# Performance work log

Hardware: AMD Instinct MI355X
Metric: run time of the kernel (lower is better)

Reference implementation:

```python
import jax, jax.numpy as jnp
import numpy as np

B, P1, P2 = 32, 25, 24          # batch, patch rows (+1 cls row), patch cols
D1, D2, D3 = 8, 8, 12           # factored embed dims (total d = 768)
H1, H2, H3 = 2, 2, 4            # factored heads (16 total)
X, Y, Z = D1 // H1, D2 // H2, D3 // H3   # per-head factor dims -> head dim 48
SCALE = float((X * Y * Z) ** -0.5)


def tle(x, w1, w2, w3, b):
    # Tensor Linear Embedding: mode-wise linear maps on the last 3 modes + bias.
    return jnp.einsum('bpqijk,ai,cj,dk->bpqacd', x, w1, w2, w3) + b


def split_heads(t):
    # (b,p1,p2,(x h1),(y h2),(z h3)) -> (b,h1,h2,h3, p1*p2, x*y*z)
    b, p1, p2, _, _, _ = t.shape
    t = t.reshape(b, p1, p2, X, H1, Y, H2, Z, H3)
    t = t.transpose(0, 4, 6, 8, 1, 2, 3, 5, 7)
    return t.reshape(b, H1, H2, H3, p1 * p2, X * Y * Z)


def merge_heads(t, p1, p2):
    # (b,h1,h2,h3,S,D) -> (b,p1,p2,(x h1),(y h2),(z h3))
    b = t.shape[0]
    t = t.reshape(b, H1, H2, H3, p1, p2, X, Y, Z)
    t = t.transpose(0, 4, 5, 6, 1, 7, 2, 8, 3)
    return t.reshape(b, p1, p2, X * H1, Y * H2, Z * H3)


def setup_inputs() -> dict:
    key = jax.random.key(0)
    ks = jax.random.split(key, 20)

    def w(k, shape):
        return jax.random.normal(k, shape, jnp.float32) * 0.02

    inp = {"x": jax.random.normal(ks[0], (B, P1, P2, D1, D2, D3), jnp.float32)}
    for i, n in enumerate(["q", "k", "v", "o"]):
        inp[f"w{n}1"] = w(ks[1 + 4 * i], (D1, D1))
        inp[f"w{n}2"] = w(ks[2 + 4 * i], (D2, D2))
        inp[f"w{n}3"] = w(ks[3 + 4 * i], (D3, D3))
        inp[f"b{n}"] = w(ks[4 + 4 * i], (D1, D2, D3))
    return inp


def reference(x, wq1, wq2, wq3, bq, wk1, wk2, wk3, bk,
              wv1, wv2, wv3, bv, wo1, wo2, wo3, bo):
    q = split_heads(tle(x, wq1, wq2, wq3, bq))
    k = split_heads(tle(x, wk1, wk2, wk3, bk))
    v = split_heads(tle(x, wv1, wv2, wv3, bv))
    # scores: (b,h1,h2,h3,S,S) with S = 600
    attn = jax.nn.softmax(jnp.einsum('befgsd,befgtd->befgst', q, k) * SCALE, axis=-1)
    o = jnp.einsum('befgst,befgtd->befgsd', attn, v)
    o = merge_heads(o, P1, P2)
    return tle(o, wo1, wo2, wo3, bo)
```

## Files before the change

kernel.cpp:

```cpp
#include <hip/hip_runtime.h>
#include <hip/hip_bf16.h>
#include <cstdint>

#define Bc    32
#define Sc    600
#define NHc   16
#define SP    640
#define NKT   19
#define DHc   48
#define DP    64
#define QW    48
#define SCALEc 0.14433756729740643f

typedef __bf16    bf16x8 __attribute__((ext_vector_type(8)));
typedef float     f32x4  __attribute__((ext_vector_type(4)));
typedef float     f32x16 __attribute__((ext_vector_type(16)));
typedef uint32_t  u32x4  __attribute__((ext_vector_type(4)));
typedef _Float16  f16x2  __attribute__((ext_vector_type(2)));

static __device__ __forceinline__ f32x4 mfma16(bf16x8 a, bf16x8 b, f32x4 c) {
    return __builtin_amdgcn_mfma_f32_16x16x32_bf16(a, b, c, 0, 0, 0);
}
static __device__ __forceinline__ f32x16 mfma32(bf16x8 a, bf16x8 b, f32x16 c) {
    return __builtin_amdgcn_mfma_f32_32x32x16_bf16(a, b, c, 0, 0, 0);
}
static __device__ __forceinline__ float fdot2u(uint32_t a, uint32_t b, float c) {
    return __builtin_amdgcn_fdot2(__builtin_bit_cast(f16x2, a),
                                  __builtin_bit_cast(f16x2, b), c, false);
}
static __device__ __forceinline__ f32x16 fzero16() {
    f32x16 z;
    #pragma unroll
    for (int i = 0; i < 16; ++i) z[i] = 0.f;
    return z;
}
static __device__ __forceinline__ void gload_lds16(const void* g, void* l) {
    __builtin_amdgcn_global_load_lds(
        (const __attribute__((address_space(1))) unsigned int*)g,
        (__attribute__((address_space(3))) unsigned int*)l, 16, 0, 0);
}
static __device__ __forceinline__ void lds_fence() {
    asm volatile("s_waitcnt lgkmcnt(0)" ::: "memory");
}

__global__ __launch_bounds__(256, 3) void tle_qkv(
    const float* __restrict__ x,
    const float* __restrict__ wq1, const float* __restrict__ wq2,
    const float* __restrict__ wq3, const float* __restrict__ bq,
    const float* __restrict__ wk1, const float* __restrict__ wk2,
    const float* __restrict__ wk3, const float* __restrict__ bk,
    const float* __restrict__ wv1, const float* __restrict__ wv2,
    const float* __restrict__ wv3, const float* __restrict__ bv,
    __hip_bfloat16* __restrict__ Qb, __hip_bfloat16* __restrict__ Kb,
    __hip_bfloat16* __restrict__ Vr)
{
    __shared__ __align__(16) char uni[16*864*2];
    unsigned short* xb  = (unsigned short*)uni;
    unsigned short* t2s = (unsigned short*)uni;
    const int t = threadIdx.x;
    const int patch0 = blockIdx.x * 16;

    {
        const int pl = t >> 4, ij0 = (t & 15) * 4;
        const float4* xg = (const float4*)(x + (size_t)(patch0 + pl) * 768 + ij0*12);
        float vv[4][12];
        #pragma unroll
        for (int ij = 0; ij < 4; ++ij) {
            float4 a = xg[ij*3+0], b = xg[ij*3+1], c = xg[ij*3+2];
            vv[ij][0]=a.x; vv[ij][1]=a.y; vv[ij][2]=a.z;  vv[ij][3]=a.w;
            vv[ij][4]=b.x; vv[ij][5]=b.y; vv[ij][6]=b.z;  vv[ij][7]=b.w;
            vv[ij][8]=c.x; vv[ij][9]=c.y; vv[ij][10]=c.z; vv[ij][11]=c.w;
        }
        #pragma unroll
        for (int k = 0; k < 12; ++k) {
            uint32_t lo, hi;
            asm("v_cvt_pk_bf16_f32 %0, %1, %2" : "=v"(lo) : "v"(vv[0][k]), "v"(vv[1][k]));
            asm("v_cvt_pk_bf16_f32 %0, %1, %2" : "=v"(hi) : "v"(vv[2][k]), "v"(vv[3][k]));
            *(uint2*)&xb[pl*864 + k*72 + ij0] = make_uint2(lo, hi);
        }
    }
    lds_fence();

    const int l = t & 63, w = t >> 6;
    const int r16 = l & 15, g = l >> 4;

    bf16x8 Bf[3][2];
    int pl_c[3], k_c[3];
    #pragma unroll
    for (int n = 0; n < 3; ++n) {
        int col = n*16 + r16;
        int pp = col / 12, kk = col - pp*12;
        pl_c[n] = w*4 + pp; k_c[n] = kk;
        #pragma unroll
        for (int kh = 0; kh < 2; ++kh)
            Bf[n][kh] = *(const bf16x8*)&xb[pl_c[n]*864 + kk*72 + kh*32 + g*8];
    }
    lds_fence();

    const int plo = t >> 4, h = t & 15;
    const int h1 = h >> 3, h2 = (h >> 2) & 1, h3 = h & 3;
    const int patch3 = patch0 + plo;
    const int b3 = patch3 / Sc, s3 = patch3 - b3*Sc;

    #pragma unroll 1
    for (int pr = 0; pr < 3; ++pr) {
        const float* w1 = pr == 0 ? wq1 : pr == 1 ? wk1 : wv1;
        const float* w2 = pr == 0 ? wq2 : pr == 1 ? wk2 : wv2;
        float w2r[8];
        #pragma unroll
        for (int j = 0; j < 8; ++j) w2r[j] = w2[(r16 & 7)*8 + j];
        bf16x8 Af[4][2];
        #pragma unroll
        for (int m = 0; m < 4; ++m) {
            int a = 2*m + (r16 >> 3);
            #pragma unroll
            for (int kh = 0; kh < 2; ++kh) {
                float w1v = w1[a*8 + kh*4 + g];
                uint32_t wd[4];
                #pragma unroll
                for (int q = 0; q < 4; ++q)
                    asm("v_cvt_pk_bf16_f32 %0, %1, %2" : "=v"(wd[q])
                        : "v"(w1v*w2r[2*q]), "v"(w1v*w2r[2*q+1]));
                Af[m][kh] = __builtin_bit_cast(bf16x8, (u32x4){wd[0],wd[1],wd[2],wd[3]});
            }
        }
        f32x4 acc[4][3];
        #pragma unroll
        for (int m = 0; m < 4; ++m)
            #pragma unroll
            for (int n = 0; n < 3; ++n) acc[m][n] = f32x4{0.f,0.f,0.f,0.f};
        #pragma unroll
        for (int m = 0; m < 4; ++m)
            #pragma unroll
            for (int n = 0; n < 3; ++n) {
                acc[m][n] = mfma16(Af[m][0], Bf[n][0], acc[m][n]);
                acc[m][n] = mfma16(Af[m][1], Bf[n][1], acc[m][n]);
            }
        #pragma unroll
        for (int m = 0; m < 4; ++m)
            #pragma unroll
            for (int n = 0; n < 3; ++n)
                #pragma unroll
                for (int r = 0; r < 4; ++r) {
                    int ac = m*16 + g*4 + r;
                    _Float16 hv = (_Float16)acc[m][n][r];
                    t2s[pl_c[n]*864 + ac*12 + k_c[n]] =
                        __builtin_bit_cast(unsigned short, hv);
                }
        lds_fence();

        const float* w3 = pr == 0 ? wq3 : pr == 1 ? wk3 : wv3;
        const float* bb = pr == 0 ? bq  : pr == 1 ? bk  : bv;
        uint32_t w3p[3][6];
        #pragma unroll
        for (int z = 0; z < 3; ++z) {
            const float* wr = w3 + (z*4 + h3)*12;
            #pragma unroll
            for (int q = 0; q < 6; ++q)
                w3p[z][q] = __builtin_bit_cast(uint32_t,
                    __builtin_amdgcn_cvt_pkrtz(wr[2*q], wr[2*q+1]));
        }
        __hip_bfloat16* dst = pr == 0 ? Qb : pr == 1 ? Kb : Vr;
        const int pitch = pr == 0 ? QW : DP;
        unsigned short* drow = (unsigned short*)dst
            + ((size_t)(b3*NHc + h) * SP + s3) * pitch;
        #pragma unroll
        for (int half = 0; half < 2; ++half) {
            float od[24];
            #pragma unroll
            for (int xh = 0; xh < 2; ++xh) {
                int xq = half*2 + xh;
                #pragma unroll
                for (int yq = 0; yq < 4; ++yq) {
                    int a = xq*2 + h1, c = yq*2 + h2;
                    int ac = a*8 + c;
                    const uint2* tp = (const uint2*)&t2s[plo*864 + ac*12];
                    uint2 q0 = tp[0], q1 = tp[1], q2 = tp[2];
                    const float* bp = bb + a*96 + c*12 + h3;
                    #pragma unroll
                    for (int z = 0; z < 3; ++z) {
                        float a3 = bp[z*4];
                        a3 = fdot2u(q0.x, w3p[z][0], a3);
                        a3 = fdot2u(q0.y, w3p[z][1], a3);
                        a3 = fdot2u(q1.x, w3p[z][2], a3);
                        a3 = fdot2u(q1.y, w3p[z][3], a3);
                        a3 = fdot2u(q2.x, w3p[z][4], a3);
                        a3 = fdot2u(q2.y, w3p[z][5], a3);
                        od[xh*12 + yq*3 + z] = a3;
                    }
                }
            }
            if (pr == 0) {
                #pragma unroll
                for (int i2 = 0; i2 < 24; ++i2) od[i2] *= SCALEc;
            }
            #pragma unroll
            for (int u = 0; u < 3; ++u) {
                uint32_t wd[4];
                #pragma unroll
                for (int q = 0; q < 4; ++q)
                    asm("v_cvt_pk_bf16_f32 %0, %1, %2" : "=v"(wd[q])
                        : "v"(od[u*8 + 2*q]), "v"(od[u*8 + 2*q + 1]));
                *(uint4*)(drow + (half*3 + u)*8) = make_uint4(wd[0], wd[1], wd[2], wd[3]);
            }
        }
        lds_fence();
    }
}

__global__ __launch_bounds__(256) void vtrans(
    const __hip_bfloat16* __restrict__ Vr, __hip_bfloat16* __restrict__ Vt,
    __hip_bfloat16* __restrict__ Kb)
{
    __shared__ __align__(16) short Ls[64][72];
    const int t = threadIdx.x;
    const int bh = blockIdx.x, st = blockIdx.y;
    const __hip_bfloat16* src = Vr + ((size_t)bh * SP + st*64) * DP;
    for (int u = t; u < 512; u += 256) {
        int r = u >> 3, c = (u & 7) * 8;
        *(bf16x8*)&Ls[r][c] = *(const bf16x8*)(src + (size_t)r * DP + c);
    }
    __syncthreads();
    const unsigned short one_bf = 0x3F80;
    for (int u = t; u < 384; u += 256) {
        int dh = u >> 3, cb = (u & 7) * 8;
        int gcol = st*64 + cb;
        if (gcol >= Sc + 8) continue;
        union { unsigned short s[8]; bf16x8 v; } o;
        if (gcol >= Sc) {
            #pragma unroll
            for (int j = 0; j < 8; ++j) o.s[j] = 0;
        } else {
            #pragma unroll
            for (int j = 0; j < 8; ++j) o.s[j] = (unsigned short)Ls[cb + j][dh];
        }
        *(bf16x8*)(Vt + ((size_t)bh*64 + dh) * SP + st*64 + cb) = o.v;
    }
    if (t < 128) {
        int r = 48 + (t >> 3), cb = (t & 7) * 8;
        union { unsigned short s[8]; bf16x8 v; } o;
        #pragma unroll
        for (int j = 0; j < 8; ++j) {
            int col = st*64 + cb + j;
            o.s[j] = (r == 48 && col < Sc) ? one_bf : (unsigned short)0;
        }
        *(bf16x8*)(Vt + ((size_t)bh*64 + r) * SP + st*64 + cb) = o.v;
    }
    if (st == 9 && t < 64) {
        int r = 600 + (t >> 3), cb = (t & 7) * 8;
        union { unsigned short s[8]; bf16x8 v; } z;
        #pragma unroll
        for (int j = 0; j < 8; ++j) z.s[j] = 0;
        *(bf16x8*)(Kb + ((size_t)bh * SP + r) * DP + cb) = z.v;
    }
}

static __device__ __forceinline__ void softmax_pack(
    const f32x16& sv, bf16x8& pf0, bf16x8& pf1)
{
    float p[16];
    #pragma unroll
    for (int r = 0; r < 16; ++r) p[r] = __expf(sv[r]);
    uint32_t Wa0, Wa1, Wa2, Wa3, Wb0, Wb1, Wb2, Wb3;
    asm("v_cvt_pk_bf16_f32 %0, %1, %2" : "=v"(Wa0) : "v"(p[0]),  "v"(p[1]));
    asm("v_cvt_pk_bf16_f32 %0, %1, %2" : "=v"(Wb0) : "v"(p[2]),  "v"(p[3]));
    asm("v_cvt_pk_bf16_f32 %0, %1, %2" : "=v"(Wa1) : "v"(p[4]),  "v"(p[5]));
    asm("v_cvt_pk_bf16_f32 %0, %1, %2" : "=v"(Wb1) : "v"(p[6]),  "v"(p[7]));
    asm("v_cvt_pk_bf16_f32 %0, %1, %2" : "=v"(Wa2) : "v"(p[8]),  "v"(p[9]));
    asm("v_cvt_pk_bf16_f32 %0, %1, %2" : "=v"(Wb2) : "v"(p[10]), "v"(p[11]));
    asm("v_cvt_pk_bf16_f32 %0, %1, %2" : "=v"(Wa3) : "v"(p[12]), "v"(p[13]));
    asm("v_cvt_pk_bf16_f32 %0, %1, %2" : "=v"(Wb3) : "v"(p[14]), "v"(p[15]));
    asm("v_permlane32_swap_b32 %0, %1" : "+v"(Wa0), "+v"(Wa1));
    asm("v_permlane32_swap_b32 %0, %1" : "+v"(Wb0), "+v"(Wb1));
    asm("v_permlane32_swap_b32 %0, %1" : "+v"(Wa2), "+v"(Wa3));
    asm("v_permlane32_swap_b32 %0, %1" : "+v"(Wb2), "+v"(Wb3));
    pf0 = __builtin_bit_cast(bf16x8, (u32x4){Wa0, Wb0, Wa1, Wb1});
    pf1 = __builtin_bit_cast(bf16x8, (u32x4){Wa2, Wb2, Wa3, Wb3});
}

__global__ __launch_bounds__(64, 2) void attn_mfma(
    const __hip_bfloat16* __restrict__ Qb, const __hip_bfloat16* __restrict__ Kb,
    const __hip_bfloat16* __restrict__ Vt, float* __restrict__ Ob)
{
    __shared__ __align__(16) char Ks[2][4096];
    __shared__ __align__(16) char Vs[2][4096];
    const int l = threadIdx.x;
    const int q32 = l & 31, hl = l >> 5;
    const int bid = blockIdx.x;
    const int lg = (bid & 7) * 320 + (bid >> 3);
    const int bh = lg / 5, qb = lg - bh * 5;
    const int b = bh >> 4, h = bh & 15;

    const char* Kbh = (const char*)(Kb + (size_t)bh * SP * DP);
    const char* Vbh = (const char*)(Vt + (size_t)bh * 64 * SP);

    const int krow = l >> 3;
    const char* ksrc = Kbh + krow*128 + (((l & 7)*16) ^ (krow << 4));
    const char* vsrc = Vbh + (size_t)(l >> 2)*(SP*2) + (l & 3)*16;

    bf16x8 qf[4][3];
    #pragma unroll
    for (int f = 0; f < 4; ++f) {
        const __hip_bfloat16* Qp = Qb + ((size_t)bh*SP + qb*128 + f*32 + q32) * QW;
        #pragma unroll
        for (int ck = 0; ck < 3; ++ck)
            qf[f][ck] = *(const bf16x8*)(Qp + ck*16 + hl*8);
    }
    f32x16 acc[4][2];
    #pragma unroll
    for (int f = 0; f < 4; ++f) { acc[f][0] = fzero16(); acc[f][1] = fzero16(); }

    auto stage = [&](int kt, int bfi) {
        const char* ks = ksrc + (size_t)kt * 4096;
        const char* vs = vsrc + (size_t)kt * 64;
        #pragma unroll
        for (int i = 0; i < 4; ++i)
            gload_lds16(ks + i*1024, &Ks[bfi][i*1024]);
        #pragma unroll
        for (int i = 0; i < 4; ++i)
            gload_lds16(vs + (size_t)i*16*(SP*2), &Vs[bfi][i*1024]);
    };

    stage(0, 0);
    int bfi = 0;
    #pragma unroll 1
    for (int kt = 0; kt < NKT; ++kt) {
        asm volatile("s_waitcnt vmcnt(0)" ::: "memory");
        __builtin_amdgcn_sched_barrier(0);
        bf16x8 kf[3], vf[2][2];
        #pragma unroll
        for (int ck = 0; ck < 3; ++ck)
            kf[ck] = *(const bf16x8*)&Ks[bfi][q32*128 + ((ck*32 + hl*16) ^ ((q32 & 7) << 4))];
        #pragma unroll
        for (int db = 0; db < 2; ++db)
            #pragma unroll
            for (int c2 = 0; c2 < 2; ++c2)
                vf[db][c2] = *(const bf16x8*)&Vs[bfi][(db*32 + q32)*64 + c2*32 + hl*16];
        if (kt + 1 < NKT) stage(kt + 1, bfi ^ 1);
        __builtin_amdgcn_s_setprio(1);
        #pragma unroll
        for (int f = 0; f < 4; ++f) {
            f32x16 s = fzero16();
            s = mfma32(kf[0], qf[f][0], s);
            s = mfma32(kf[1], qf[f][1], s);
            s = mfma32(kf[2], qf[f][2], s);
            bf16x8 pf0, pf1;
            softmax_pack(s, pf0, pf1);
            acc[f][0] = mfma32(vf[0][0], pf0, acc[f][0]);
            acc[f][0] = mfma32(vf[0][1], pf1, acc[f][0]);
            acc[f][1] = mfma32(vf[1][0], pf0, acc[f][1]);
            acc[f][1] = mfma32(vf[1][1], pf1, acc[f][1]);
        }
        __builtin_amdgcn_s_setprio(0);
        bfi ^= 1;
    }

    #pragma unroll
    for (int f = 0; f < 4; ++f) {
        float ls = acc[f][1][8];
        float other = __shfl_xor(ls, 32);
        float tot = hl ? other : ls;
        float inv = 1.f / tot;
        int q = qb*128 + f*32 + q32;
        if (q < Sc) {
            float* orow = Ob + ((size_t)b*Sc + q)*768 + h*48;
            #pragma unroll
            for (int rq = 0; rq < 4; ++rq) {
                int d0 = rq*8 + hl*4;
                float4 v4 = make_float4(acc[f][0][rq*4+0]*inv, acc[f][0][rq*4+1]*inv,
                                        acc[f][0][rq*4+2]*inv, acc[f][0][rq*4+3]*inv);
                *(float4*)(orow + d0) = v4;
            }
            #pragma unroll
            for (int rq = 0; rq < 2; ++rq) {
                int d0 = 32 + rq*8 + hl*4;
                float4 v4 = make_float4(acc[f][1][rq*4+0]*inv, acc[f][1][rq*4+1]*inv,
                                        acc[f][1][rq*4+2]*inv, acc[f][1][rq*4+3]*inv);
                *(float4*)(orow + d0) = v4;
            }
        }
    }
}

__global__ __launch_bounds__(256, 3) void tle_out(
    const float* __restrict__ Oin, const float* __restrict__ w1g,
    const float* __restrict__ w2g, const float* __restrict__ w3g,
    const float* __restrict__ bias, float* __restrict__ out)
{
    __shared__ __align__(16) float xs[4][768];
    __shared__ __align__(16) unsigned short t1s[4][8][104];
    const int t = threadIdx.x;
    const int p = t >> 6, a = (t >> 3) & 7, c = t & 7;
    const int lane = t & 63;
    const int patch = blockIdx.x * 4 + p;
    for (int o4 = lane; o4 < 192; o4 += 64) {
        float4 v = *(const float4*)(Oin + (size_t)patch * 768 + o4*4);
        int h = o4 / 12, r = o4 - h*12;
        #pragma unroll
        for (int q = 0; q < 4; ++q) {
            int dh = r*4 + q;
            int xq = dh / 12, rem2 = dh - xq*12, yq = rem2 / 3, zq = rem2 - yq*3;
            int aa = xq*2 + (h >> 3), cc = yq*2 + ((h >> 2) & 1), dd = zq*4 + (h & 3);
            xs[p][aa*96 + cc*12 + dd] = ((const float*)&v)[q];
        }
    }
    float w1r[8], w2r[8];
    #pragma unroll
    for (int i = 0; i < 8; ++i) { w1r[i] = w1g[a*8 + i]; w2r[i] = w2g[c*8 + i]; }
    lds_fence();

    float s1[12];
    #pragma unroll
    for (int k = 0; k < 12; ++k) s1[k] = 0.f;
    #pragma unroll
    for (int i = 0; i < 8; ++i) {
        const float4* xr = (const float4*)&xs[p][i*96 + c*12];
        float4 v0 = xr[0], v1 = xr[1], v2 = xr[2];
        float wv = w1r[i];
        s1[0] += wv*v0.x; s1[1] += wv*v0.y; s1[2]  += wv*v0.z; s1[3]  += wv*v0.w;
        s1[4] += wv*v1.x; s1[5] += wv*v1.y; s1[6]  += wv*v1.z; s1[7]  += wv*v1.w;
        s1[8] += wv*v2.x; s1[9] += wv*v2.y; s1[10] += wv*v2.z; s1[11] += wv*v2.w;
    }
    {
        uint32_t pk[6];
        #pragma unroll
        for (int n = 0; n < 6; ++n)
            asm("v_cvt_pk_bf16_f32 %0, %1, %2" : "=v"(pk[n])
                : "v"(s1[2*n]), "v"(s1[2*n+1]));
        unsigned short* row = &t1s[p][a][0];
        *(uint2*)(row + c*12 + 0) = make_uint2(pk[0], pk[1]);
        *(uint2*)(row + c*12 + 4) = make_uint2(pk[2], pk[3]);
        *(uint2*)(row + c*12 + 8) = make_uint2(pk[4], pk[5]);
    }
    lds_fence();

    uint4 q[12];
    const uint4* t1p = (const uint4*)&t1s[p][a][0];
    #pragma unroll
    for (int n = 0; n < 12; ++n) q[n] = t1p[n];
    float t2r[12];
    #pragma unroll
    for (int k = 0; k < 12; ++k) t2r[k] = 0.f;
    #pragma unroll
    for (int j = 0; j < 8; ++j) {
        float wv = w2r[j];
        #pragma unroll
        for (int k = 0; k < 12; ++k) {
            int idx = j*12 + k;
            uint32_t ww = __builtin_bit_cast(u32x4, q[idx >> 3])[(idx >> 1) & 3];
            float xv = __builtin_bit_cast(float,
                (idx & 1) ? (ww & 0xffff0000u) : (ww << 16));
            t2r[k] += wv * xv;
        }
    }
    const float4* bp = (const float4*)(bias + a*96 + c*12);
    float4 b0 = bp[0], b1 = bp[1], b2 = bp[2];
    float bias_[12] = {b0.x,b0.y,b0.z,b0.w, b1.x,b1.y,b1.z,b1.w, b2.x,b2.y,b2.z,b2.w};
    float od[12];
    #pragma unroll
    for (int d = 0; d < 12; ++d) {
        const float4* wr = (const float4*)(w3g + d*12);
        float4 u0 = wr[0], u1 = wr[1], u2 = wr[2];
        od[d] = bias_[d]
            + t2r[0]*u0.x + t2r[1]*u0.y + t2r[2] *u0.z + t2r[3] *u0.w
            + t2r[4]*u1.x + t2r[5]*u1.y + t2r[6] *u1.z + t2r[7] *u1.w
            + t2r[8]*u2.x + t2r[9]*u2.y + t2r[10]*u2.z + t2r[11]*u2.w;
    }
    float4* op = (float4*)(out + (size_t)patch*768 + a*96 + c*12);
    op[0] = make_float4(od[0], od[1], od[2],  od[3]);
    op[1] = make_float4(od[4], od[5], od[6],  od[7]);
    op[2] = make_float4(od[8], od[9], od[10], od[11]);
}

extern "C" void kernel_launch(void* const* d_in, const int* in_sizes, int n_in,
                              void* d_out, int out_size, void* d_ws, size_t ws_size,
                              hipStream_t stream) {
    const float* x   = (const float*)d_in[0];
    const float* wq1 = (const float*)d_in[1];
    const float* wq2 = (const float*)d_in[2];
    const float* wq3 = (const float*)d_in[3];
    const float* bq  = (const float*)d_in[4];
    const float* wk1 = (const float*)d_in[5];
    const float* wk2 = (const float*)d_in[6];
    const float* wk3 = (const float*)d_in[7];
    const float* bk  = (const float*)d_in[8];
    const float* wv1 = (const float*)d_in[9];
    const float* wv2 = (const float*)d_in[10];
    const float* wv3 = (const float*)d_in[11];
    const float* bv  = (const float*)d_in[12];
    const float* wo1 = (const float*)d_in[13];
    const float* wo2 = (const float*)d_in[14];
    const float* wo3 = (const float*)d_in[15];
    const float* bo  = (const float*)d_in[16];
    float* out = (float*)d_out;

    char* ws = (char*)d_ws;
    const size_t SZ_Q = (size_t)512 * SP * QW * 2;
    const size_t SZ_K = (size_t)512 * SP * DP * 2;
    __hip_bfloat16* Qb = (__hip_bfloat16*)ws;
    __hip_bfloat16* Kb = (__hip_bfloat16*)(ws + SZ_Q);
    __hip_bfloat16* Vr = (__hip_bfloat16*)(ws + SZ_Q + SZ_K);
    __hip_bfloat16* Vt = (__hip_bfloat16*)(ws + SZ_Q + 2*SZ_K);
    float*          Ob = (float*)(ws + SZ_Q + 3*SZ_K);

    tle_qkv<<<Bc*Sc/16, 256, 0, stream>>>(x, wq1, wq2, wq3, bq,
                                          wk1, wk2, wk3, bk,
                                          wv1, wv2, wv3, bv, Qb, Kb, Vr);
    vtrans<<<dim3(512, 10), 256, 0, stream>>>(Vr, Vt, Kb);
    attn_mfma<<<2560, 64, 0, stream>>>(Qb, Kb, Vt, Ob);
    tle_out<<<Bc*Sc/4, 256, 0, stream>>>(Ob, wo1, wo2, wo3, bo, out);
}
```

Measured before the change: 161.9 us.

## Precompute packed QKV weight fragments in prep kernel and swizzle V tile LDS layout

Adds a small prep kernel that builds, once per call, the bf16 W1⊗W2 MFMA fragments, the fp16-packed W3 rows and a head-reordered bias, with the softmax scale folded into the Q weights and bias. Every tle_qkv block then loads these instead of rebuilding them from fp32 weights and scaling Q afterwards. It also XOR-swizzles the V tile addresses in the attention kernel's LDS staging and reads to cut bank conflicts. The cost is an extra kernel launch and more workspace; folding the scale before bf16 rounding slightly changes numerics.

After: 169.4 us. 4.6% more time.

```diff
diff --git a/kernel.cpp b/kernel.cpp
--- a/kernel.cpp
+++ b/kernel.cpp
@@ -42,15 +42,58 @@
 static __device__ __forceinline__ void lds_fence() {
     asm volatile("s_waitcnt lgkmcnt(0)" ::: "memory");
 }
-
-__global__ __launch_bounds__(256, 3) void tle_qkv(
-    const float* __restrict__ x,
+static __device__ __forceinline__ uint32_t pkbf(float a, float b) {
+    uint32_t r;
+    asm("v_cvt_pk_bf16_f32 %0, %1, %2" : "=v"(r) : "v"(a), "v"(b));
+    return r;
+}
+
+__global__ __launch_bounds__(256) void prep(
     const float* __restrict__ wq1, const float* __restrict__ wq2,
     const float* __restrict__ wq3, const float* __restrict__ bq,
     const float* __restrict__ wk1, const float* __restrict__ wk2,
     const float* __restrict__ wk3, const float* __restrict__ bk,
     const float* __restrict__ wv1, const float* __restrict__ wv2,
     const float* __restrict__ wv3, const float* __restrict__ bv,
+    __hip_bfloat16* __restrict__ W12f, float* __restrict__ biasr,
+    uint32_t* __restrict__ w3f)
+{
+    const int pr = blockIdx.x, t = threadIdx.x;
+    const float* w1 = pr == 0 ? wq1 : pr == 1 ? wk1 : wv1;
+    const float* w2 = pr == 0 ? wq2 : pr == 1 ? wk2 : wv2;
+    const float* w3 = pr == 0 ? wq3 : pr == 1 ? wk3 : wv3;
+    const float* bb = pr == 0 ? bq  : pr == 1 ? bk  : bv;
+    const float sc = pr == 0 ? SCALEc : 1.f;
+
+    for (int grp = t; grp < 512; grp += 256) {
+        int mkh = grp >> 6, lane = grp & 63;
+        int m = mkh >> 1, kh = mkh & 1;
+        int g = lane >> 4, r16 = lane & 15;
+        float w1v = sc * w1[(2*m + (r16 >> 3))*8 + kh*4 + g];
+        uint32_t wd[4];
+        #pragma unroll
+        for (int q = 0; q < 4; ++q)
+            wd[q] = pkbf(w1v * w2[(r16 & 7)*8 + 2*q], w1v * w2[(r16 & 7)*8 + 2*q + 1]);
+        *(uint4*)((unsigned short*)W12f + ((size_t)pr*512 + grp)*8)
+            = make_uint4(wd[0], wd[1], wd[2], wd[3]);
+    }
+    for (int idx = t; idx < 768; idx += 256) {
+        int h = idx / 48, dh = idx - h*48;
+        int xq = dh / 12, r2 = dh - xq*12, yq = r2 / 3, z = r2 - yq*3;
+        int a = xq*2 + (h >> 3), c = yq*2 + ((h >> 2) & 1), d = z*4 + (h & 3);
+        biasr[(size_t)pr*768 + idx] = sc * bb[a*96 + c*12 + d];
+    }
+    if (t < 72) {
+        int d = t / 6, q = t - d*6;
+        w3f[((size_t)pr*12 + d)*8 + q] = __builtin_bit_cast(uint32_t,
+            __builtin_amdgcn_cvt_pkrtz(w3[d*12 + 2*q], w3[d*12 + 2*q + 1]));
+    }
+}
+
+__global__ __launch_bounds__(256, 3) void tle_qkv(
+    const float* __restrict__ x,
+    const __hip_bfloat16* __restrict__ W12f, const float* __restrict__ biasr,
+    const uint32_t* __restrict__ w3f,
     __hip_bfloat16* __restrict__ Qb, __hip_bfloat16* __restrict__ Kb,
     __hip_bfloat16* __restrict__ Vr)
 {
@@ -73,9 +116,8 @@
         }
         #pragma unroll
         for (int k = 0; k < 12; ++k) {
-            uint32_t lo, hi;
-            asm("v_cvt_pk_bf16_f32 %0, %1, %2" : "=v"(lo) : "v"(vv[0][k]), "v"(vv[1][k]));
-            asm("v_cvt_pk_bf16_f32 %0, %1, %2" : "=v"(hi) : "v"(vv[2][k]), "v"(vv[3][k]));
+            uint32_t lo = pkbf(vv[0][k], vv[1][k]);
+            uint32_t hi = pkbf(vv[2][k], vv[3][k]);
             *(uint2*)&xb[pl*864 + k*72 + ij0] = make_uint2(lo, hi);
         }
     }
@@ -98,32 +140,19 @@
     lds_fence();
 
     const int plo = t >> 4, h = t & 15;
-    const int h1 = h >> 3, h2 = (h >> 2) & 1, h3 = h & 3;
+    const int h3 = h & 3;
     const int patch3 = patch0 + plo;
     const int b3 = patch3 / Sc, s3 = patch3 - b3*Sc;
+    const bf16x8* W12p = (const bf16x8*)W12f;
 
     #pragma unroll 1
     for (int pr = 0; pr < 3; ++pr) {
-        const float* w1 = pr == 0 ? wq1 : pr == 1 ? wk1 : wv1;
-        const float* w2 = pr == 0 ? wq2 : pr == 1 ? wk2 : wv2;
-        float w2r[8];
-        #pragma unroll
-        for (int j = 0; j < 8; ++j) w2r[j] = w2[(r16 & 7)*8 + j];
         bf16x8 Af[4][2];
         #pragma unroll
-        for (int m = 0; m < 4; ++m) {
-            int a = 2*m + (r16 >> 3);
-            #pragma unroll
-            for (int kh = 0; kh < 2; ++kh) {
-                float w1v = w1[a*8 + kh*4 + g];
-                uint32_t wd[4];
-                #pragma unroll
-                for (int q = 0; q < 4; ++q)
-                    asm("v_cvt_pk_bf16_f32 %0, %1, %2" : "=v"(wd[q])
-                        : "v"(w1v*w2r[2*q]), "v"(w1v*w2r[2*q+1]));
-                Af[m][kh] = __builtin_bit_cast(bf16x8, (u32x4){wd[0],wd[1],wd[2],wd[3]});
-            }
-        }
+        for (int m = 0; m < 4; ++m)
+            #pragma unroll
+            for (int kh = 0; kh < 2; ++kh)
+                Af[m][kh] = W12p[((size_t)pr*8 + m*2 + kh)*64 + l];
         f32x4 acc[4][3];
         #pragma unroll
         for (int m = 0; m < 4; ++m)
@@ -149,17 +178,16 @@
                 }
         lds_fence();
 
-        const float* w3 = pr == 0 ? wq3 : pr == 1 ? wk3 : wv3;
-        const float* bb = pr == 0 ? bq  : pr == 1 ? bk  : bv;
         uint32_t w3p[3][6];
         #pragma unroll
         for (int z = 0; z < 3; ++z) {
-            const float* wr = w3 + (z*4 + h3)*12;
-            #pragma unroll
-            for (int q = 0; q < 6; ++q)
-                w3p[z][q] = __builtin_bit_cast(uint32_t,
-                    __builtin_amdgcn_cvt_pkrtz(wr[2*q], wr[2*q+1]));
-        }
+            const uint32_t* wr = w3f + ((size_t)pr*12 + z*4 + h3)*8;
+            uint4 wa = *(const uint4*)wr;
+            uint2 wb = *(const uint2*)(wr + 4);
+            w3p[z][0]=wa.x; w3p[z][1]=wa.y; w3p[z][2]=wa.z; w3p[z][3]=wa.w;
+            w3p[z][4]=wb.x; w3p[z][5]=wb.y;
+        }
+        const float4* brow = (const float4*)(biasr + ((size_t)pr*16 + h)*48);
         __hip_bfloat16* dst = pr == 0 ? Qb : pr == 1 ? Kb : Vr;
         const int pitch = pr == 0 ? QW : DP;
         unsigned short* drow = (unsigned short*)dst
@@ -168,18 +196,22 @@
         for (int half = 0; half < 2; ++half) {
             float od[24];
             #pragma unroll
+            for (int j = 0; j < 6; ++j) {
+                float4 bv = brow[half*6 + j];
+                od[j*4+0]=bv.x; od[j*4+1]=bv.y; od[j*4+2]=bv.z; od[j*4+3]=bv.w;
+            }
+            #pragma unroll
             for (int xh = 0; xh < 2; ++xh) {
                 int xq = half*2 + xh;
                 #pragma unroll
                 for (int yq = 0; yq < 4; ++yq) {
-                    int a = xq*2 + h1, c = yq*2 + h2;
+                    int a = xq*2 + (h >> 3), c = yq*2 + ((h >> 2) & 1);
                     int ac = a*8 + c;
                     const uint2* tp = (const uint2*)&t2s[plo*864 + ac*12];
                     uint2 q0 = tp[0], q1 = tp[1], q2 = tp[2];
-                    const float* bp = bb + a*96 + c*12 + h3;
                     #pragma unroll
                     for (int z = 0; z < 3; ++z) {
-                        float a3 = bp[z*4];
+                        float a3 = od[xh*12 + yq*3 + z];
                         a3 = fdot2u(q0.x, w3p[z][0], a3);
                         a3 = fdot2u(q0.y, w3p[z][1], a3);
                         a3 = fdot2u(q1.x, w3p[z][2], a3);
@@ -190,17 +222,12 @@
                     }
                 }
             }
-            if (pr == 0) {
-                #pragma unroll
-                for (int i2 = 0; i2 < 24; ++i2) od[i2] *= SCALEc;
-            }
             #pragma unroll
             for (int u = 0; u < 3; ++u) {
                 uint32_t wd[4];
                 #pragma unroll
                 for (int q = 0; q < 4; ++q)
-                    asm("v_cvt_pk_bf16_f32 %0, %1, %2" : "=v"(wd[q])
-                        : "v"(od[u*8 + 2*q]), "v"(od[u*8 + 2*q + 1]));
+                    wd[q] = pkbf(od[u*8 + 2*q], od[u*8 + 2*q + 1]);
                 *(uint4*)(drow + (half*3 + u)*8) = make_uint4(wd[0], wd[1], wd[2], wd[3]);
             }
         }
@@ -262,14 +289,10 @@
     #pragma unroll
     for (int r = 0; r < 16; ++r) p[r] = __expf(sv[r]);
     uint32_t Wa0, Wa1, Wa2, Wa3, Wb0, Wb1, Wb2, Wb3;
-    asm("v_cvt_pk_bf16_f32 %0, %1, %2" : "=v"(Wa0) : "v"(p[0]),  "v"(p[1]));
-    asm("v_cvt_pk_bf16_f32 %0, %1, %2" : "=v"(Wb0) : "v"(p[2]),  "v"(p[3]));
-    asm("v_cvt_pk_bf16_f32 %0, %1, %2" : "=v"(Wa1) : "v"(p[4]),  "v"(p[5]));
-    asm("v_cvt_pk_bf16_f32 %0, %1, %2" : "=v"(Wb1) : "v"(p[6]),  "v"(p[7]));
-    asm("v_cvt_pk_bf16_f32 %0, %1, %2" : "=v"(Wa2) : "v"(p[8]),  "v"(p[9]));
-    asm("v_cvt_pk_bf16_f32 %0, %1, %2" : "=v"(Wb2) : "v"(p[10]), "v"(p[11]));
-    asm("v_cvt_pk_bf16_f32 %0, %1, %2" : "=v"(Wa3) : "v"(p[12]), "v"(p[13]));
-    asm("v_cvt_pk_bf16_f32 %0, %1, %2" : "=v"(Wb3) : "v"(p[14]), "v"(p[15]));
+    Wa0 = pkbf(p[0], p[1]);   Wb0 = pkbf(p[2], p[3]);
+    Wa1 = pkbf(p[4], p[5]);   Wb1 = pkbf(p[6], p[7]);
+    Wa2 = pkbf(p[8], p[9]);   Wb2 = pkbf(p[10], p[11]);
+    Wa3 = pkbf(p[12], p[13]); Wb3 = pkbf(p[14], p[15]);
     asm("v_permlane32_swap_b32 %0, %1" : "+v"(Wa0), "+v"(Wa1));
     asm("v_permlane32_swap_b32 %0, %1" : "+v"(Wb0), "+v"(Wb1));
     asm("v_permlane32_swap_b32 %0, %1" : "+v"(Wa2), "+v"(Wa3));
@@ -296,7 +319,8 @@
 
     const int krow = l >> 3;
     const char* ksrc = Kbh + krow*128 + (((l & 7)*16) ^ (krow << 4));
-    const char* vsrc = Vbh + (size_t)(l >> 2)*(SP*2) + (l & 3)*16;
+    const char* vsrc = Vbh + (size_t)(l >> 2)*(SP*2)
+                     + (((l & 3) ^ ((l >> 3) & 3)) * 16);
 
     bf16x8 qf[4][3];
     #pragma unroll
@@ -335,7 +359,8 @@
         for (int db = 0; db < 2; ++db)
             #pragma unroll
             for (int c2 = 0; c2 < 2; ++c2)
-                vf[db][c2] = *(const bf16x8*)&Vs[bfi][(db*32 + q32)*64 + c2*32 + hl*16];
+                vf[db][c2] = *(const bf16x8*)&Vs[bfi][(db*32 + q32)*64
+                                + ((c2*32 + hl*16) ^ (((q32 >> 1) & 3) << 4))];
         if (kt + 1 < NKT) stage(kt + 1, bfi ^ 1);
         __builtin_amdgcn_s_setprio(1);
         #pragma unroll
@@ -424,9 +449,7 @@
     {
         uint32_t pk[6];
         #pragma unroll
-        for (int n = 0; n < 6; ++n)
-            asm("v_cvt_pk_bf16_f32 %0, %1, %2" : "=v"(pk[n])
-                : "v"(s1[2*n]), "v"(s1[2*n+1]));
+        for (int n = 0; n < 6; ++n) pk[n] = pkbf(s1[2*n], s1[2*n+1]);
         unsigned short* row = &t1s[p][a][0];
         *(uint2*)(row + c*12 + 0) = make_uint2(pk[0], pk[1]);
         *(uint2*)(row + c*12 + 4) = make_uint2(pk[2], pk[3]);
@@ -495,17 +518,22 @@
     float* out = (float*)d_out;
 
     char* ws = (char*)d_ws;
-    const size_t SZ_Q = (size_t)512 * SP * QW * 2;
-    const size_t SZ_K = (size_t)512 * SP * DP * 2;
+    const size_t SZ_Q  = (size_t)512 * SP * QW * 2;
+    const size_t SZ_K  = (size_t)512 * SP * DP * 2;
+    const size_t SZ_OB = (size_t)32 * 600 * 768 * 4;
     __hip_bfloat16* Qb = (__hip_bfloat16*)ws;
     __hip_bfloat16* Kb = (__hip_bfloat16*)(ws + SZ_Q);
     __hip_bfloat16* Vr = (__hip_bfloat16*)(ws + SZ_Q + SZ_K);
     __hip_bfloat16* Vt = (__hip_bfloat16*)(ws + SZ_Q + 2*SZ_K);
     float*          Ob = (float*)(ws + SZ_Q + 3*SZ_K);
-
-    tle_qkv<<<Bc*Sc/16, 256, 0, stream>>>(x, wq1, wq2, wq3, bq,
-                                          wk1, wk2, wk3, bk,
-                                          wv1, wv2, wv3, bv, Qb, Kb, Vr);
+    char* tb = ws + SZ_Q + 3*SZ_K + SZ_OB;
+    __hip_bfloat16* W12f  = (__hip_bfloat16*)tb;
+    float*          biasr = (float*)(tb + 24576);
+    uint32_t*       w3f   = (uint32_t*)(tb + 24576 + 9216);
+
+    prep<<<3, 256, 0, stream>>>(wq1, wq2, wq3, bq, wk1, wk2, wk3, bk,
+                                wv1, wv2, wv3, bv, W12f, biasr, w3f);
+    tle_qkv<<<Bc*Sc/16, 256, 0, stream>>>(x, W12f, biasr, w3f, Qb, Kb, Vr);
     vtrans<<<dim3(512, 10), 256, 0, stream>>>(Vr, Vt, Kb);
     attn_mfma<<<2560, 64, 0, stream>>>(Qb, Kb, Vt, Ob);
     tle_out<<<Bc*Sc/4, 256, 0, stream>>>(Ob, wo1, wo2, wo3, bo, out);
```
